# Performance work log

Measured on AMD Instinct MI355X. Metric: run time of the kernel, lower is better.

Reference implementation:

```python
import jax, jax.numpy as jnp
import numpy as np

N_NODES = 10000
D_FEAT = 128
N_EDGES = 640000


def setup_inputs() -> dict:
    key = jax.random.key(0)
    k1, k2, k3, k4, k5 = jax.random.split(key, 5)
    feat = jax.random.normal(k1, (N_NODES, D_FEAT), dtype=jnp.float32)
    # fc_pool: Linear(D_FEAT, D_FEAT) as in DGL SAGEConv pool aggregator
    W_pool = jax.random.normal(k2, (D_FEAT, D_FEAT), dtype=jnp.float32) / jnp.sqrt(D_FEAT)
    b_pool = jax.random.normal(k3, (D_FEAT,), dtype=jnp.float32) * 0.01
    edge_src = jax.random.randint(k4, (N_EDGES,), 0, N_NODES, dtype=jnp.int32)
    edge_dst = jax.random.randint(k5, (N_EDGES,), 0, N_NODES, dtype=jnp.int32)
    return {"feat": feat, "W_pool": W_pool, "b_pool": b_pool,
            "edge_src": edge_src, "edge_dst": edge_dst}


def reference(feat, W_pool, b_pool, edge_src, edge_dst):
    # feat_drop is identity (p=0 / eval mode)
    # h = relu(fc_pool(feat_src))  -> [N, D]
    h = jax.nn.relu(feat @ W_pool + b_pool)
    # copy_src + fn.max: per-destination max over incoming edge messages
    msgs = h[edge_src]                                   # [E, D] gather
    neigh = jax.ops.segment_max(msgs, edge_dst, num_segments=N_NODES)
    # zero-in-degree nodes get 0 (DGL convention); since msgs >= 0 post-relu,
    # clamping at 0 only affects empty segments (which are -inf).
    neigh = jnp.maximum(neigh, 0.0)
    # pooling_residual: h_neigh + feat_dst
    return neigh + feat
```

## Files before the change

kernel.cpp:

```cpp
#include <hip/hip_runtime.h>
#include <hip/hip_bf16.h>

#define N_NODES 10000
#define D_FEAT 128
#define N_EDGES 640000
#define NB 128
#define EPB 5000
#define CAP 128

__global__ __launch_bounds__(256) void gemm_relu_kernel(
    const float* __restrict__ feat, const float* __restrict__ W,
    const float* __restrict__ b, unsigned* __restrict__ h_u) {
  __shared__ float fs[8][D_FEAT];
  const int t = threadIdx.x;
  const int row0 = blockIdx.x * 8;
  ((float4*)&fs[0][0])[t] = ((const float4*)(feat + row0 * D_FEAT))[t];
  __syncthreads();

  const int c4 = t & 31;
  const int r  = t >> 5;
  const float4* __restrict__ W4 = (const float4*)W;
  float4 acc = make_float4(0.f, 0.f, 0.f, 0.f);
#pragma unroll 8
  for (int k = 0; k < D_FEAT; ++k) {
    const float f = fs[r][k];
    const float4 w = W4[k * 32 + c4];
    acc.x += f * w.x; acc.y += f * w.y; acc.z += f * w.z; acc.w += f * w.w;
  }
  const float4 bb = ((const float4*)b)[c4];
  float v0 = fmaxf(acc.x + bb.x, 0.f);
  float v1 = fmaxf(acc.y + bb.y, 0.f);
  float v2 = fmaxf(acc.z + bb.z, 0.f);
  float v3 = fmaxf(acc.w + bb.w, 0.f);
  __hip_bfloat162 p0 = __float22bfloat162_rn(make_float2(v0, v1));
  __hip_bfloat162 p1 = __float22bfloat162_rn(make_float2(v2, v3));
  uint2 u;
  u.x = *reinterpret_cast<unsigned*>(&p0);
  u.y = *reinterpret_cast<unsigned*>(&p1);
  ((uint2*)h_u)[(row0 + r) * 32 + c4] = u;
}

__global__ __launch_bounds__(256) void hist_kernel(
    const int4* __restrict__ dst4, unsigned* __restrict__ bh) {
  __shared__ unsigned cnt[N_NODES];
  const int t = threadIdx.x;
  const int b = blockIdx.x;
  for (int i = t; i < N_NODES; i += 256) cnt[i] = 0u;
  __syncthreads();
  const int base4 = b * (EPB / 4);
#pragma unroll
  for (int q = 0; q < 5; ++q) {
    const int i = q * 256 + t;
    if (i < EPB / 4) {
      const int4 d = dst4[base4 + i];
      atomicAdd(&cnt[d.x], 1u); atomicAdd(&cnt[d.y], 1u);
      atomicAdd(&cnt[d.z], 1u); atomicAdd(&cnt[d.w], 1u);
    }
  }
  __syncthreads();
  unsigned* __restrict__ row = bh + (size_t)b * N_NODES;
  for (int i = t; i < N_NODES; i += 256) row[i] = cnt[i];
}

__global__ __launch_bounds__(256) void colscan_kernel(
    unsigned* __restrict__ bh, unsigned* __restrict__ cnt_total) {
  const int d = blockIdx.x * 256 + threadIdx.x;
  if (d >= N_NODES) return;
  unsigned run = 0;
#pragma unroll 8
  for (int b = 0; b < NB; ++b) {
    const size_t idx = (size_t)b * N_NODES + d;
    const unsigned v = bh[idx];
    bh[idx] = run;
    run += v;
  }
  cnt_total[d] = run;
}

__global__ __launch_bounds__(256) void scatter_kernel(
    const int4* __restrict__ src4, const int4* __restrict__ dst4,
    const unsigned* __restrict__ bh, unsigned* __restrict__ elist) {
  __shared__ unsigned cnt[N_NODES];
  const int t = threadIdx.x;
  const int b = blockIdx.x;
  for (int i = t; i < N_NODES; i += 256) cnt[i] = 0u;
  __syncthreads();
  const unsigned* __restrict__ row = bh + (size_t)b * N_NODES;
  const int base4 = b * (EPB / 4);
#pragma unroll
  for (int q = 0; q < 5; ++q) {
    const int i = q * 256 + t;
    if (i < EPB / 4) {
      const int4 s = src4[base4 + i];
      const int4 d = dst4[base4 + i];
      unsigned p;
      p = atomicAdd(&cnt[d.x], 1u) + row[d.x]; if (p < CAP) elist[((unsigned)d.x << 7) + p] = (unsigned)s.x;
      p = atomicAdd(&cnt[d.y], 1u) + row[d.y]; if (p < CAP) elist[((unsigned)d.y << 7) + p] = (unsigned)s.y;
      p = atomicAdd(&cnt[d.z], 1u) + row[d.z]; if (p < CAP) elist[((unsigned)d.z << 7) + p] = (unsigned)s.z;
      p = atomicAdd(&cnt[d.w], 1u) + row[d.w]; if (p < CAP) elist[((unsigned)d.w << 7) + p] = (unsigned)s.w;
    }
  }
}

__device__ __forceinline__ void accum_bf16(unsigned u, float& lo, float& hi) {
  lo = fmaxf(lo, __uint_as_float(u << 16));
  hi = fmaxf(hi, __uint_as_float(u & 0xffff0000u));
}

__global__ __launch_bounds__(128) void aggregate_kernel(
    const uint4* __restrict__ h16, const float4* __restrict__ feat4,
    const unsigned* __restrict__ cnt_total, const unsigned* __restrict__ elist,
    float4* __restrict__ out4) {
  const int d = blockIdx.x;
  const int t = threadIdx.x;
  const int slot8 = t >> 4;
  const int j = t & 15;

  __shared__ unsigned sl[CAP];
  __shared__ float red[16][8];

  const unsigned n = min(cnt_total[d], (unsigned)CAP);
  if ((unsigned)t < n) sl[t] = elist[((unsigned)d << 7) + (unsigned)t];
  __syncthreads();

  float m0 = 0.f, m1 = 0.f, m2 = 0.f, m3 = 0.f,
        m4 = 0.f, m5 = 0.f, m6 = 0.f, m7 = 0.f;
  unsigned bpos = 0;
  for (; bpos + 16 <= n; bpos += 16) {
    const unsigned sA = sl[bpos + slot8];
    const unsigned sB = sl[bpos + 8 + slot8];
    const uint4 qA = h16[sA * 16 + j];
    const uint4 qB = h16[sB * 16 + j];
    accum_bf16(qA.x, m0, m1); accum_bf16(qA.y, m2, m3);
    accum_bf16(qA.z, m4, m5); accum_bf16(qA.w, m6, m7);
    accum_bf16(qB.x, m0, m1); accum_bf16(qB.y, m2, m3);
    accum_bf16(qB.z, m4, m5); accum_bf16(qB.w, m6, m7);
  }
  for (; bpos < n; bpos += 8) {
    if (bpos + slot8 < n) {
      const uint4 q = h16[sl[bpos + slot8] * 16 + j];
      accum_bf16(q.x, m0, m1); accum_bf16(q.y, m2, m3);
      accum_bf16(q.z, m4, m5); accum_bf16(q.w, m6, m7);
    }
  }

  m0 = fmaxf(m0, __shfl_xor(m0, 16)); m1 = fmaxf(m1, __shfl_xor(m1, 16));
  m2 = fmaxf(m2, __shfl_xor(m2, 16)); m3 = fmaxf(m3, __shfl_xor(m3, 16));
  m4 = fmaxf(m4, __shfl_xor(m4, 16)); m5 = fmaxf(m5, __shfl_xor(m5, 16));
  m6 = fmaxf(m6, __shfl_xor(m6, 16)); m7 = fmaxf(m7, __shfl_xor(m7, 16));
  m0 = fmaxf(m0, __shfl_xor(m0, 32)); m1 = fmaxf(m1, __shfl_xor(m1, 32));
  m2 = fmaxf(m2, __shfl_xor(m2, 32)); m3 = fmaxf(m3, __shfl_xor(m3, 32));
  m4 = fmaxf(m4, __shfl_xor(m4, 32)); m5 = fmaxf(m5, __shfl_xor(m5, 32));
  m6 = fmaxf(m6, __shfl_xor(m6, 32)); m7 = fmaxf(m7, __shfl_xor(m7, 32));

  if (t >= 64 && t < 80) {
    red[t - 64][0] = m0; red[t - 64][1] = m1; red[t - 64][2] = m2; red[t - 64][3] = m3;
    red[t - 64][4] = m4; red[t - 64][5] = m5; red[t - 64][6] = m6; red[t - 64][7] = m7;
  }
  __syncthreads();
  if (t < 16) {
    m0 = fmaxf(m0, red[t][0]); m1 = fmaxf(m1, red[t][1]);
    m2 = fmaxf(m2, red[t][2]); m3 = fmaxf(m3, red[t][3]);
    m4 = fmaxf(m4, red[t][4]); m5 = fmaxf(m5, red[t][5]);
    m6 = fmaxf(m6, red[t][6]); m7 = fmaxf(m7, red[t][7]);
    const float4 fA = feat4[d * 32 + t * 2];
    const float4 fB = feat4[d * 32 + t * 2 + 1];
    out4[d * 32 + t * 2]     = make_float4(m0 + fA.x, m1 + fA.y, m2 + fA.z, m3 + fA.w);
    out4[d * 32 + t * 2 + 1] = make_float4(m4 + fB.x, m5 + fB.y, m6 + fB.z, m7 + fB.w);
  }
}

extern "C" void kernel_launch(void* const* d_in, const int* in_sizes, int n_in,
                              void* d_out, int out_size, void* d_ws, size_t ws_size,
                              hipStream_t stream) {
  const float* feat   = (const float*)d_in[0];
  const float* W_pool = (const float*)d_in[1];
  const float* b_pool = (const float*)d_in[2];
  const int* edge_src = (const int*)d_in[3];
  const int* edge_dst = (const int*)d_in[4];
  float* out = (float*)d_out;

  char* ws = (char*)d_ws;
  unsigned* h_u       = (unsigned*)(ws);
  unsigned* bh        = (unsigned*)(ws + 2560000);
  unsigned* cnt_total = (unsigned*)(ws + 7680000);
  unsigned* elist     = (unsigned*)(ws + 7720064);

  gemm_relu_kernel<<<N_NODES / 8, 256, 0, stream>>>(feat, W_pool, b_pool, h_u);
  hist_kernel<<<NB, 256, 0, stream>>>((const int4*)edge_dst, bh);
  colscan_kernel<<<(N_NODES + 255) / 256, 256, 0, stream>>>(bh, cnt_total);
  scatter_kernel<<<NB, 256, 0, stream>>>(
      (const int4*)edge_src, (const int4*)edge_dst, bh, elist);
  aggregate_kernel<<<N_NODES, 128, 0, stream>>>(
      (const uint4*)h_u, (const float4*)feat, cnt_total, elist, (float4*)out);
}
```

Measured before the change: 128.0 us.

## Fuse histogram, scan and scatter into one kernel using global atomic offsets

Replaces the per-block histogram, column prefix-scan and scatter kernels with one kernel. It builds a per-block shared histogram, reserves global slots per destination with one atomicAdd, then scatters the edges. Zeroing of the global counters is folded into the GEMM kernel, and NB doubles. The aggregate loop is unrolled to four gathers in flight, and the residual feat load is issued before the sync. This removes two launches and the 5 MB histogram round trip. In exchange, edge order within a segment becomes nondeterministic, and the kernel uses 80 KB of LDS per block.

```diff
diff --git a/kernel.cpp b/kernel.cpp
--- a/kernel.cpp
+++ b/kernel.cpp
@@ -4,15 +4,19 @@
 #define N_NODES 10000
 #define D_FEAT 128
 #define N_EDGES 640000
-#define NB 128
-#define EPB 5000
+#define NB 256
+#define EPB 2500
 #define CAP 128
 
 __global__ __launch_bounds__(256) void gemm_relu_kernel(
     const float* __restrict__ feat, const float* __restrict__ W,
-    const float* __restrict__ b, unsigned* __restrict__ h_u) {
+    const float* __restrict__ b, unsigned* __restrict__ h_u,
+    unsigned* __restrict__ gcnt) {
   __shared__ float fs[8][D_FEAT];
   const int t = threadIdx.x;
+  const int gid = blockIdx.x * 256 + t;
+  if (gid < N_NODES) gcnt[gid] = 0u;
+
   const int row0 = blockIdx.x * 8;
   ((float4*)&fs[0][0])[t] = ((const float4*)(feat + row0 * D_FEAT))[t];
   __syncthreads();
@@ -40,65 +44,37 @@
   ((uint2*)h_u)[(row0 + r) * 32 + c4] = u;
 }
 
-__global__ __launch_bounds__(256) void hist_kernel(
-    const int4* __restrict__ dst4, unsigned* __restrict__ bh) {
+__global__ __launch_bounds__(256) void sortscatter_kernel(
+    const int* __restrict__ edge_src, const int* __restrict__ edge_dst,
+    unsigned* __restrict__ gcnt, unsigned* __restrict__ elist) {
   __shared__ unsigned cnt[N_NODES];
+  __shared__ unsigned base[N_NODES];
   const int t = threadIdx.x;
   const int b = blockIdx.x;
   for (int i = t; i < N_NODES; i += 256) cnt[i] = 0u;
   __syncthreads();
-  const int base4 = b * (EPB / 4);
-#pragma unroll
-  for (int q = 0; q < 5; ++q) {
-    const int i = q * 256 + t;
-    if (i < EPB / 4) {
-      const int4 d = dst4[base4 + i];
-      atomicAdd(&cnt[d.x], 1u); atomicAdd(&cnt[d.y], 1u);
-      atomicAdd(&cnt[d.z], 1u); atomicAdd(&cnt[d.w], 1u);
-    }
+
+  const int4* __restrict__ src4 = (const int4*)(edge_src + b * EPB);
+  const int4* __restrict__ dst4 = (const int4*)(edge_dst + b * EPB);
+  for (int i = t; i < EPB / 4; i += 256) {
+    const int4 d = dst4[i];
+    atomicAdd(&cnt[d.x], 1u); atomicAdd(&cnt[d.y], 1u);
+    atomicAdd(&cnt[d.z], 1u); atomicAdd(&cnt[d.w], 1u);
   }
   __syncthreads();
-  unsigned* __restrict__ row = bh + (size_t)b * N_NODES;
-  for (int i = t; i < N_NODES; i += 256) row[i] = cnt[i];
-}
-
-__global__ __launch_bounds__(256) void colscan_kernel(
-    unsigned* __restrict__ bh, unsigned* __restrict__ cnt_total) {
-  const int d = blockIdx.x * 256 + threadIdx.x;
-  if (d >= N_NODES) return;
-  unsigned run = 0;
-#pragma unroll 8
-  for (int b = 0; b < NB; ++b) {
-    const size_t idx = (size_t)b * N_NODES + d;
-    const unsigned v = bh[idx];
-    bh[idx] = run;
-    run += v;
+  for (int i = t; i < N_NODES; i += 256) {
+    const unsigned c = cnt[i];
+    if (c) { base[i] = atomicAdd(&gcnt[i], c); cnt[i] = 0u; }
   }
-  cnt_total[d] = run;
-}
-
-__global__ __launch_bounds__(256) void scatter_kernel(
-    const int4* __restrict__ src4, const int4* __restrict__ dst4,
-    const unsigned* __restrict__ bh, unsigned* __restrict__ elist) {
-  __shared__ unsigned cnt[N_NODES];
-  const int t = threadIdx.x;
-  const int b = blockIdx.x;
-  for (int i = t; i < N_NODES; i += 256) cnt[i] = 0u;
   __syncthreads();
-  const unsigned* __restrict__ row = bh + (size_t)b * N_NODES;
-  const int base4 = b * (EPB / 4);
-#pragma unroll
-  for (int q = 0; q < 5; ++q) {
-    const int i = q * 256 + t;
-    if (i < EPB / 4) {
-      const int4 s = src4[base4 + i];
-      const int4 d = dst4[base4 + i];
-      unsigned p;
-      p = atomicAdd(&cnt[d.x], 1u) + row[d.x]; if (p < CAP) elist[((unsigned)d.x << 7) + p] = (unsigned)s.x;
-      p = atomicAdd(&cnt[d.y], 1u) + row[d.y]; if (p < CAP) elist[((unsigned)d.y << 7) + p] = (unsigned)s.y;
-      p = atomicAdd(&cnt[d.z], 1u) + row[d.z]; if (p < CAP) elist[((unsigned)d.z << 7) + p] = (unsigned)s.z;
-      p = atomicAdd(&cnt[d.w], 1u) + row[d.w]; if (p < CAP) elist[((unsigned)d.w << 7) + p] = (unsigned)s.w;
-    }
+  for (int i = t; i < EPB / 4; i += 256) {
+    const int4 s = src4[i];
+    const int4 d = dst4[i];
+    unsigned p;
+    p = atomicAdd(&cnt[d.x], 1u) + base[d.x]; if (p < CAP) elist[((unsigned)d.x << 7) + p] = (unsigned)s.x;
+    p = atomicAdd(&cnt[d.y], 1u) + base[d.y]; if (p < CAP) elist[((unsigned)d.y << 7) + p] = (unsigned)s.y;
+    p = atomicAdd(&cnt[d.z], 1u) + base[d.z]; if (p < CAP) elist[((unsigned)d.z << 7) + p] = (unsigned)s.z;
+    p = atomicAdd(&cnt[d.w], 1u) + base[d.w]; if (p < CAP) elist[((unsigned)d.w << 7) + p] = (unsigned)s.w;
   }
 }
 
@@ -109,7 +85,7 @@
 
 __global__ __launch_bounds__(128) void aggregate_kernel(
     const uint4* __restrict__ h16, const float4* __restrict__ feat4,
-    const unsigned* __restrict__ cnt_total, const unsigned* __restrict__ elist,
+    const unsigned* __restrict__ gcnt, const unsigned* __restrict__ elist,
     float4* __restrict__ out4) {
   const int d = blockIdx.x;
   const int t = threadIdx.x;
@@ -119,22 +95,35 @@
   __shared__ unsigned sl[CAP];
   __shared__ float red[16][8];
 
-  const unsigned n = min(cnt_total[d], (unsigned)CAP);
+  const unsigned n = min(gcnt[d], (unsigned)CAP);
   if ((unsigned)t < n) sl[t] = elist[((unsigned)d << 7) + (unsigned)t];
+  float4 fA, fB;
+  if (t < 16) {
+    fA = feat4[d * 32 + t * 2];
+    fB = feat4[d * 32 + t * 2 + 1];
+  }
   __syncthreads();
 
   float m0 = 0.f, m1 = 0.f, m2 = 0.f, m3 = 0.f,
         m4 = 0.f, m5 = 0.f, m6 = 0.f, m7 = 0.f;
   unsigned bpos = 0;
-  for (; bpos + 16 <= n; bpos += 16) {
+  for (; bpos + 32 <= n; bpos += 32) {
     const unsigned sA = sl[bpos + slot8];
     const unsigned sB = sl[bpos + 8 + slot8];
+    const unsigned sC = sl[bpos + 16 + slot8];
+    const unsigned sD = sl[bpos + 24 + slot8];
     const uint4 qA = h16[sA * 16 + j];
     const uint4 qB = h16[sB * 16 + j];
+    const uint4 qC = h16[sC * 16 + j];
+    const uint4 qD = h16[sD * 16 + j];
     accum_bf16(qA.x, m0, m1); accum_bf16(qA.y, m2, m3);
     accum_bf16(qA.z, m4, m5); accum_bf16(qA.w, m6, m7);
     accum_bf16(qB.x, m0, m1); accum_bf16(qB.y, m2, m3);
     accum_bf16(qB.z, m4, m5); accum_bf16(qB.w, m6, m7);
+    accum_bf16(qC.x, m0, m1); accum_bf16(qC.y, m2, m3);
+    accum_bf16(qC.z, m4, m5); accum_bf16(qC.w, m6, m7);
+    accum_bf16(qD.x, m0, m1); accum_bf16(qD.y, m2, m3);
+    accum_bf16(qD.z, m4, m5); accum_bf16(qD.w, m6, m7);
   }
   for (; bpos < n; bpos += 8) {
     if (bpos + slot8 < n) {
@@ -163,8 +152,6 @@
     m2 = fmaxf(m2, red[t][2]); m3 = fmaxf(m3, red[t][3]);
     m4 = fmaxf(m4, red[t][4]); m5 = fmaxf(m5, red[t][5]);
     m6 = fmaxf(m6, red[t][6]); m7 = fmaxf(m7, red[t][7]);
-    const float4 fA = feat4[d * 32 + t * 2];
-    const float4 fB = feat4[d * 32 + t * 2 + 1];
     out4[d * 32 + t * 2]     = make_float4(m0 + fA.x, m1 + fA.y, m2 + fA.z, m3 + fA.w);
     out4[d * 32 + t * 2 + 1] = make_float4(m4 + fB.x, m5 + fB.y, m6 + fB.z, m7 + fB.w);
   }
@@ -181,16 +168,12 @@
   float* out = (float*)d_out;
 
   char* ws = (char*)d_ws;
-  unsigned* h_u       = (unsigned*)(ws);
-  unsigned* bh        = (unsigned*)(ws + 2560000);
-  unsigned* cnt_total = (unsigned*)(ws + 7680000);
-  unsigned* elist     = (unsigned*)(ws + 7720064);
+  unsigned* h_u   = (unsigned*)(ws);
+  unsigned* gcnt  = (unsigned*)(ws + 2560000);
+  unsigned* elist = (unsigned*)(ws + 2600064);
 
-  gemm_relu_kernel<<<N_NODES / 8, 256, 0, stream>>>(feat, W_pool, b_pool, h_u);
-  hist_kernel<<<NB, 256, 0, stream>>>((const int4*)edge_dst, bh);
-  colscan_kernel<<<(N_NODES + 255) / 256, 256, 0, stream>>>(bh, cnt_total);
-  scatter_kernel<<<NB, 256, 0, stream>>>(
-      (const int4*)edge_src, (const int4*)edge_dst, bh, elist);
+  gemm_relu_kernel<<<N_NODES / 8, 256, 0, stream>>>(feat, W_pool, b_pool, h_u, gcnt);
+  sortscatter_kernel<<<NB, 256, 0, stream>>>(edge_src, edge_dst, gcnt, elist);
   aggregate_kernel<<<N_NODES, 128, 0, stream>>>(
-      (const uint4*)h_u, (const float4*)feat, cnt_total, elist, (float4*)out);
+      (const uint4*)h_u, (const float4*)feat, gcnt, elist, (float4*)out);
 }
```

Measured after the change: 131.8 us. 3.0% more time.
